# Kernel tuning notes

Hardware: AMD Instinct MI355X
Metric: run time of the kernel (lower is better)

Reference implementation:

```python
import jax, jax.numpy as jnp
import numpy as np

NSIDE = 64
NLAT = 4 * NSIDE - 1        # 255 iso-latitude rings
NLON = 4 * NSIDE            # 256 = max pixels per ring
NPIX = 12 * NSIDE * NSIDE   # 49152 HEALPix pixels
LMAX = NLAT                 # 255
MMAX = NLON // 2 + 1        # 129
BATCH, CHAN = 8, 32


def _ring_geometry():
    # HEALPix ring scheme: ring r (0-based), 1-based i=r+1
    #  north cap i<nside: nph=4i, phi shift 0.5
    #  equatorial nside<=i<=3*nside: nph=4*nside, shift alternates {0,0.5}
    #  south cap: mirror of north cap
    nph = np.zeros(NLAT, np.int64)
    shift = np.zeros(NLAT, np.float64)
    for r in range(NLAT):
        i = r + 1
        if i < NSIDE:
            nph[r], shift[r] = 4 * i, 0.5
        elif i <= 3 * NSIDE:
            nph[r], shift[r] = 4 * NSIDE, 0.5 * ((i - NSIDE + 1) % 2)
        else:
            nph[r], shift[r] = 4 * (NLAT - r), 0.5
    offs = np.concatenate([[0], np.cumsum(nph)[:-1]])
    p = np.arange(NLON)
    mask = (p[None, :] < nph[:, None])                       # [nlat, nlon]
    idx = (offs[:, None] + p[None, :]) * mask                # padded -> 0
    phase = 2.0 * np.pi * (p[None, :] + shift[:, None]) / nph[:, None] * mask
    return idx.astype(np.int32), mask.astype(np.float32), phase.astype(np.float32)


def setup_inputs() -> dict:
    key = jax.random.key(0)
    k1, k2, k3 = jax.random.split(key, 3)
    idx, mask, phase = _ring_geometry()
    x = jax.random.normal(k1, (BATCH, CHAN, NPIX), jnp.float32)
    pct = jax.random.normal(k2, (MMAX, LMAX, NLAT), jnp.float32) * 0.1  # Legendre table stand-in
    w = jax.random.uniform(k3, (NLAT,), jnp.float32)                    # per-ring quadrature weights
    return {"x": x, "pct": pct, "w": w,
            "ring_index": jnp.asarray(idx),
            "ring_mask": jnp.asarray(mask),
            "phase": jnp.asarray(phase)}


def _healpix_rfft_real(x, ring_index, ring_mask, phase):
    # x: [..., npix] -> per-ring DFT coefficients as real pairs [..., nlat, mmax, 2]
    rings = x[..., ring_index] * ring_mask                 # [..., nlat, nlon]
    m = jnp.arange(MMAX, dtype=phase.dtype)
    ang = phase[:, :, None] * m                            # [nlat, nlon, mmax]
    fr = jnp.einsum('...kp,kpm->...km', rings, jnp.cos(ang))
    fi = -jnp.einsum('...kp,kpm->...km', rings, jnp.sin(ang))
    return jnp.stack([fr, fi], axis=-1)                    # n=2 is view_as_real axis


def reference(x, pct, w, ring_index, ring_mask, phase):
    # healpix ring rFFT, then Legendre contraction (einsum '...kmn,mlk->...lmn')
    f = _healpix_rfft_real(x, ring_index, ring_mask, phase)  # [..., nlat, mmax, 2]
    weights = pct * w                                        # [mmax, lmax, nlat]
    out = jnp.einsum('...kmn,mlk->...lmn', f, weights)       # [..., lmax, mmax, 2]
    return out
```

## Files before the change

kernel.cpp:

```cpp
#include <hip/hip_runtime.h>

#define NLAT 255
#define NLON 256
#define NPIX 49152
#define MMAX 129
#define MCS  258
#define NTBL 65
#define TROWS 264

typedef unsigned short ushort_t;
typedef __attribute__((ext_vector_type(8)))  short  bf16x8;
typedef __attribute__((ext_vector_type(4)))  short  short4v;
typedef __attribute__((ext_vector_type(16))) float  f32x16;
typedef __attribute__((ext_vector_type(4)))  float  float4v;

__device__ __forceinline__ ushort_t f2bf(float f) {
    union { float f; unsigned u; } v; v.f = f;
    unsigned r = v.u + 0x7FFFu + ((v.u >> 16) & 1u);
    return (ushort_t)(r >> 16);
}
__device__ __forceinline__ float bf2f(ushort_t h) {
    union { unsigned u; float f; } v; v.u = ((unsigned)h) << 16;
    return v.f;
}

__global__ __launch_bounds__(256) void prepK(const float* __restrict__ pct,
                                             const float* __restrict__ w,
                                             ushort_t* __restrict__ pctw) {
    const int m  = blockIdx.x;
    const int l0 = blockIdx.y * 32;
    const int t  = threadIdx.x;
    const float wk = (t < NLAT) ? w[t] : 0.f;
    for (int l = l0; l < l0 + 32; ++l) {
        float v = 0.f;
        if (l < NLAT && t < NLAT)
            v = pct[((size_t)m * NLAT + l) * NLAT + t] * wk;
        pctw[((size_t)m * 256 + l) * 256 + t] = f2bf(v);
    }
}

__global__ __launch_bounds__(256) void trigK(const float* __restrict__ phase,
                                             const float* __restrict__ mask,
                                             ushort_t* __restrict__ Ttab2) {
    const int tt  = blockIdx.x;
    const int mcs = blockIdx.y;
    const int p   = threadIdx.x;
    const int r   = (tt < 63) ? tt : (tt == 63 ? 63 : 64);
    float val = 0.f;
    if (mcs < MCS) {
        float ph = phase[r * NLON + p];
        float mk = mask[r * NLON + p];
        float fm = (float)(mcs >> 1);
        float s, c;
        __sincosf(ph * fm, &s, &c);
        val = (mcs & 1) ? (-s * mk) : (c * mk);
    }
    Ttab2[(((size_t)tt * 4 + (p >> 6)) * TROWS + mcs) * 64 + (p & 63)] = f2bf(val);
}

__global__ __launch_bounds__(512, 2) void stageA(const float* __restrict__ x,
                                                 const int* __restrict__ ring_index,
                                                 const ushort_t* __restrict__ Ttab2,
                                                 ushort_t* __restrict__ f1) {
    __shared__ __align__(16) ushort_t Rs[256 * 72];
    __shared__ __align__(16) ushort_t Ts[TROWS * 72];

    const int r  = blockIdx.x;
    const int i1 = r + 1;
    const int nph = (i1 < 64) ? 4 * i1 : (i1 <= 192 ? 256 : 4 * (256 - i1));
    const int tbl = (i1 < 64) ? r : (i1 <= 192 ? (63 + (((i1 - 63) & 1) ^ 1)) : 254 - r);
    const int base = ring_index[r * NLON];

    const int t    = threadIdx.x;
    const int lane = t & 63;
    const int wid  = t >> 6;
    const int wrow = wid >> 1, wcol = wid & 1;
    const int lg   = lane >> 5;
    const int lc   = lane & 31;

    f32x16 acc[5][2];
#pragma unroll
    for (int tau = 0; tau < 5; ++tau)
#pragma unroll
        for (int i = 0; i < 2; ++i)
#pragma unroll
            for (int q = 0; q < 16; ++q) acc[tau][i][q] = 0.f;

    for (int pc = 0; pc < nph; pc += 64) {
        {
            const int p0 = (t & 15) * 4;
            const bool ok = (pc + p0) < nph;
#pragma unroll
            for (int pass = 0; pass < 8; ++pass) {
                int bc = (t >> 4) + pass * 32;
                float4v v = {0.f, 0.f, 0.f, 0.f};
                if (ok) v = *(const float4v*)(x + (size_t)bc * NPIX + base + pc + p0);
                short4v h;
                h[0] = (short)f2bf(v[0]); h[1] = (short)f2bf(v[1]);
                h[2] = (short)f2bf(v[2]); h[3] = (short)f2bf(v[3]);
                *(short4v*)(Rs + bc * 72 + p0) = h;
            }
        }
        {
            const ushort_t* slab = Ttab2 + ((size_t)tbl * 4 + (pc >> 6)) * (TROWS * 64);
#pragma unroll
            for (int pass = 0; pass < 5; ++pass) {
                int id = t + pass * 512;
                if (id < (TROWS * 64 / 8)) {
                    bf16x8 v = *(const bf16x8*)(slab + id * 8);
                    *(bf16x8*)(Ts + (id >> 3) * 72 + (id & 7) * 8) = v;
                }
            }
        }
        __syncthreads();
#pragma unroll
        for (int ks = 0; ks < 4; ++ks) {
            bf16x8 a0 = *(const bf16x8*)(Rs + (wrow * 64 + lc) * 72 + ks * 16 + lg * 8);
            bf16x8 a1 = *(const bf16x8*)(Rs + (wrow * 64 + 32 + lc) * 72 + ks * 16 + lg * 8);
#pragma unroll
            for (int tau = 0; tau < 5; ++tau) {
                int rr = tau * 64 + wcol * 32 + lc;
                int trow = rr > (TROWS - 1) ? (TROWS - 1) : rr;
                bf16x8 b = *(const bf16x8*)(Ts + trow * 72 + ks * 16 + lg * 8);
                acc[tau][0] = __builtin_amdgcn_mfma_f32_32x32x16_bf16(a0, b, acc[tau][0], 0, 0, 0);
                acc[tau][1] = __builtin_amdgcn_mfma_f32_32x32x16_bf16(a1, b, acc[tau][1], 0, 0, 0);
            }
        }
        __syncthreads();
    }

    ushort_t* Olds = Rs;
#pragma unroll
    for (int tau = 0; tau < 5; ++tau) {
        __syncthreads();
        {
            const int mcsl = wcol * 32 + lc;
#pragma unroll
            for (int i = 0; i < 2; ++i)
#pragma unroll
                for (int q = 0; q < 16; ++q) {
                    int bc = wrow * 64 + i * 32 + 4 * lg + (q & 3) + 8 * (q >> 2);
                    Olds[mcsl * 264 + bc] = f2bf(acc[tau][i][q]);
                }
        }
        __syncthreads();
#pragma unroll
        for (int it = 0; it < 4; ++it) {
            int row = (t >> 5) + it * 16;
            int ch  = t & 31;
            int mcs = tau * 64 + row;
            if (mcs < MCS) {
                bf16x8 v = *(const bf16x8*)(Olds + row * 264 + ch * 8);
                int m = mcs >> 1, n = mcs & 1;
                *(bf16x8*)(f1 + ((size_t)m * NLAT + r) * 512 + n * 256 + ch * 8) = v;
            }
        }
    }
}

__global__ __launch_bounds__(256) void transK(const ushort_t* __restrict__ f1,
                                              ushort_t* __restrict__ f1t, int m0) {
    __shared__ __align__(16) ushort_t T[64][72];
    const int m  = m0 + blockIdx.x;
    const int k0 = blockIdx.y * 64;
    const int b0 = blockIdx.z * 64;
    const int t  = threadIdx.x;
#pragma unroll
    for (int it = 0; it < 2; ++it) {
        int id = t + it * 256;
        int kk = id >> 3, ch = id & 7;
        int k  = k0 + kk;
        bf16x8 v = {0,0,0,0,0,0,0,0};
        if (k < NLAT)
            v = *(const bf16x8*)(f1 + ((size_t)m * NLAT + k) * 512 + b0 + ch * 8);
        *(bf16x8*)(&T[kk][ch * 8]) = v;
    }
    __syncthreads();
#pragma unroll
    for (int it = 0; it < 2; ++it) {
        int id  = t + it * 256;
        int bb  = id & 63, ch8 = id >> 6;
        bf16x8 v;
#pragma unroll
        for (int j = 0; j < 8; ++j) v[j] = T[ch8 * 8 + j][bb];
        *(bf16x8*)(f1t + ((size_t)m * 512 + b0 + bb) * 256 + k0 + ch8 * 8) = v;
    }
}

__global__ __launch_bounds__(256, 2) void stageB(const ushort_t* __restrict__ f1t,
                                                 const ushort_t* __restrict__ pctw,
                                                 ushort_t* __restrict__ otmp,
                                                 int mbase) {
    __shared__ __align__(16) ushort_t SB[30720];
    ushort_t* As = SB;
    ushort_t* Ws = SB + 10240;
    ushort_t* Es = SB;

    const int m   = mbase + (blockIdx.x >> 2);
    const int sub = blockIdx.x & 3;
    const int b2t = sub * 128;

    const int t     = threadIdx.x;
    const int lane  = t & 63;
    const int wid   = t >> 6;
    const int wrow  = wid >> 1, wlcol = wid & 1;
    const int lg    = lane >> 5, lc = lane & 31;

    f32x16 acc[2][4];
#pragma unroll
    for (int i = 0; i < 2; ++i)
#pragma unroll
        for (int j = 0; j < 4; ++j)
#pragma unroll
            for (int q = 0; q < 16; ++q) acc[i][j][q] = 0.f;

    auto fillA = [&](ushort_t* dst, int kc) {
#pragma unroll
        for (int pass = 0; pass < 2; ++pass) {
            int id  = t + pass * 256;
            int row = id >> 2, ch = id & 3;
            bf16x8 v = *(const bf16x8*)(f1t + ((size_t)m * 512 + b2t + row) * 256 + kc + ch * 8);
            *(bf16x8*)(dst + row * 40 + ch * 8) = v;
        }
    };
    auto fillW = [&](ushort_t* dst, int kc) {
#pragma unroll
        for (int pass = 0; pass < 4; ++pass) {
            int id  = t + pass * 256;
            int row = id >> 2, ch = id & 3;
            bf16x8 v = *(const bf16x8*)(pctw + ((size_t)m * 256 + row) * 256 + kc + ch * 8);
            *(bf16x8*)(dst + row * 40 + ch * 8) = v;
        }
    };

    fillA(As, 0);
    fillW(Ws, 0);
    __syncthreads();
    int buf = 0;
    for (int kc = 0; kc < 256; kc += 32, buf ^= 1) {
        if (kc + 32 < 256) {
            fillA(As + (buf ^ 1) * 5120, kc + 32);
            fillW(Ws + (buf ^ 1) * 10240, kc + 32);
        }
        const ushort_t* A = As + buf * 5120;
        const ushort_t* W = Ws + buf * 10240;
#pragma unroll
        for (int ks = 0; ks < 2; ++ks) {
            const int ko = ks * 16 + lg * 8;
            bf16x8 a0 = *(const bf16x8*)(A + (wrow * 64 + lc) * 40 + ko);
            bf16x8 a1 = *(const bf16x8*)(A + (wrow * 64 + 32 + lc) * 40 + ko);
#pragma unroll
            for (int jj = 0; jj < 4; ++jj) {
                bf16x8 b = *(const bf16x8*)(W + (wlcol * 128 + jj * 32 + lc) * 40 + ko);
                acc[0][jj] = __builtin_amdgcn_mfma_f32_32x32x16_bf16(a0, b, acc[0][jj], 0, 0, 0);
                acc[1][jj] = __builtin_amdgcn_mfma_f32_32x32x16_bf16(a1, b, acc[1][jj], 0, 0, 0);
            }
        }
        __syncthreads();
    }

#pragma unroll
    for (int h = 0; h < 2; ++h) {
        if (h) __syncthreads();
        if (wlcol == h) {
#pragma unroll
            for (int i = 0; i < 2; ++i)
#pragma unroll
                for (int jj = 0; jj < 4; ++jj)
#pragma unroll
                    for (int q = 0; q < 16; ++q) {
                        int bl = wrow * 64 + i * 32 + 4 * lg + (q & 3) + 8 * (q >> 2);
                        Es[bl * 136 + jj * 32 + lc] = f2bf(acc[i][jj][q]);
                    }
        }
        __syncthreads();
#pragma unroll
        for (int it = 0; it < 8; ++it) {
            int id  = t + it * 256;
            int row = id >> 4, ch = id & 15;
            bf16x8 v = *(const bf16x8*)(Es + row * 136 + ch * 8);
            *(bf16x8*)(otmp + (((size_t)m * 512 + b2t + row) << 8) + h * 128 + ch * 8) = v;
        }
    }
}

__global__ __launch_bounds__(256) void permuteK(const ushort_t* __restrict__ otmp,
                                                float* __restrict__ out) {
    __shared__ ushort_t L[MCS * 66];
    const int bc = blockIdx.x;
    const int l0 = blockIdx.y * 64;
    const int t  = threadIdx.x;
    const int ll = t & 63;
    const int l  = l0 + ll;
#pragma unroll 4
    for (int it = 0; it < 65; ++it) {
        int mn = (t >> 6) + it * 4;
        if (mn < MCS) {
            int mm = mn >> 1, n = mn & 1;
            ushort_t v = 0;
            if (l < NLAT)
                v = otmp[(((size_t)mm * 512 + n * 256 + bc) << 8) + l];
            L[mn * 66 + ll] = v;
        }
    }
    __syncthreads();
    for (int ll2 = 0; ll2 < 64; ++ll2) {
        int lo = l0 + ll2;
        if (lo >= NLAT) break;
        size_t rowb = ((size_t)bc * NLAT + lo) * MCS;
        out[rowb + t] = bf2f(L[t * 66 + ll2]);
        if (t < 2)
            out[rowb + 256 + t] = bf2f(L[(256 + t) * 66 + ll2]);
    }
}

extern "C" void kernel_launch(void* const* d_in, const int* in_sizes, int n_in,
                              void* d_out, int out_size, void* d_ws, size_t ws_size,
                              hipStream_t stream) {
    const float* x          = (const float*)d_in[0];
    const float* pct        = (const float*)d_in[1];
    const float* w          = (const float*)d_in[2];
    const int*   ring_index = (const int*)d_in[3];
    const float* ring_mask  = (const float*)d_in[4];
    const float* phase      = (const float*)d_in[5];
    float* out = (float*)d_out;

    char* wsb = (char*)d_ws;
    ushort_t* f1    = (ushort_t*)wsb;
    ushort_t* Ttab2 = (ushort_t*)(wsb + 33684480);
    ushort_t* f1t   = (ushort_t*)(wsb + 33552384);
    ushort_t* otmp  = (ushort_t*)wsb;
    ushort_t* pctw  = (ushort_t*)d_out;

    prepK   <<<dim3(MMAX, 8),   256, 0, stream>>>(pct, w, pctw);
    trigK   <<<dim3(NTBL, TROWS), 256, 0, stream>>>(phase, ring_mask, Ttab2);
    stageA  <<<dim3(NLAT),      512, 0, stream>>>(x, ring_index, Ttab2, f1);
    transK  <<<dim3(1, 4, 8),   256, 0, stream>>>(f1, f1t, 128);
    transK  <<<dim3(128, 4, 8), 256, 0, stream>>>(f1, f1t, 0);
    stageB  <<<dim3(256),       256, 0, stream>>>(f1t, pctw, otmp, 0);
    stageB  <<<dim3(260),       256, 0, stream>>>(f1t, pctw, otmp, 64);
    permuteK<<<dim3(256, 4),    256, 0, stream>>>(otmp, out);
}
```

Before: 142.4 us.

## Split stageA across batch-channel tiles with swizzled trig table and direct LDS loads

StageA now launches 4x more blocks, each handling 64 of the 256 batch-channel rows for one ring, with 256 threads and a smaller per-block accumulator. The goal is more parallelism and occupancy beyond the 255 ring blocks. The trig table is written in an XOR-swizzled layout so it can be copied straight into LDS with global_load_lds, with no padding and no register round trip, while still avoiding bank conflicts. The cost is that each trig slab is now loaded four times, once per batch tile, which adds global and L2 traffic.

```diff
diff --git a/kernel.cpp b/kernel.cpp
--- a/kernel.cpp
+++ b/kernel.cpp
@@ -55,17 +55,20 @@
         __sincosf(ph * fm, &s, &c);
         val = (mcs & 1) ? (-s * mk) : (c * mk);
     }
-    Ttab2[(((size_t)tt * 4 + (p >> 6)) * TROWS + mcs) * 64 + (p & 63)] = f2bf(val);
-}
-
-__global__ __launch_bounds__(512, 2) void stageA(const float* __restrict__ x,
+    const int pl  = p & 63;
+    const int swz = ((((pl >> 3) ^ mcs) & 7) << 3) | (pl & 7);
+    Ttab2[(((size_t)tt * 4 + (p >> 6)) * TROWS + mcs) * 64 + swz] = f2bf(val);
+}
+
+__global__ __launch_bounds__(256, 3) void stageA(const float* __restrict__ x,
                                                  const int* __restrict__ ring_index,
                                                  const ushort_t* __restrict__ Ttab2,
                                                  ushort_t* __restrict__ f1) {
-    __shared__ __align__(16) ushort_t Rs[256 * 72];
-    __shared__ __align__(16) ushort_t Ts[TROWS * 72];
-
-    const int r  = blockIdx.x;
+    __shared__ __align__(16) ushort_t Rs[64 * 72];
+    __shared__ __align__(16) ushort_t Ts[TROWS * 64];
+
+    const int b0 = blockIdx.x * 64;
+    const int r  = blockIdx.y;
     const int i1 = r + 1;
     const int nph = (i1 < 64) ? 4 * i1 : (i1 <= 192 ? 256 : 4 * (256 - i1));
     const int tbl = (i1 < 64) ? r : (i1 <= 192 ? (63 + (((i1 - 63) & 1) ^ 1)) : 254 - r);
@@ -78,23 +81,21 @@
     const int lg   = lane >> 5;
     const int lc   = lane & 31;
 
-    f32x16 acc[5][2];
+    f32x16 acc[5];
 #pragma unroll
     for (int tau = 0; tau < 5; ++tau)
 #pragma unroll
-        for (int i = 0; i < 2; ++i)
-#pragma unroll
-            for (int q = 0; q < 16; ++q) acc[tau][i][q] = 0.f;
+        for (int q = 0; q < 16; ++q) acc[tau][q] = 0.f;
 
     for (int pc = 0; pc < nph; pc += 64) {
         {
             const int p0 = (t & 15) * 4;
             const bool ok = (pc + p0) < nph;
 #pragma unroll
-            for (int pass = 0; pass < 8; ++pass) {
-                int bc = (t >> 4) + pass * 32;
+            for (int pass = 0; pass < 4; ++pass) {
+                int bc = (t >> 4) + pass * 16;
                 float4v v = {0.f, 0.f, 0.f, 0.f};
-                if (ok) v = *(const float4v*)(x + (size_t)bc * NPIX + base + pc + p0);
+                if (ok) v = *(const float4v*)(x + (size_t)(b0 + bc) * NPIX + base + pc + p0);
                 short4v h;
                 h[0] = (short)f2bf(v[0]); h[1] = (short)f2bf(v[1]);
                 h[2] = (short)f2bf(v[2]); h[3] = (short)f2bf(v[3]);
@@ -103,27 +104,24 @@
         }
         {
             const ushort_t* slab = Ttab2 + ((size_t)tbl * 4 + (pc >> 6)) * (TROWS * 64);
-#pragma unroll
-            for (int pass = 0; pass < 5; ++pass) {
-                int id = t + pass * 512;
-                if (id < (TROWS * 64 / 8)) {
-                    bf16x8 v = *(const bf16x8*)(slab + id * 8);
-                    *(bf16x8*)(Ts + (id >> 3) * 72 + (id & 7) * 8) = v;
-                }
+            for (int s = wid; s < 33; s += 4) {
+                __builtin_amdgcn_global_load_lds(
+                    (const __attribute__((address_space(1))) void*)(slab + s * 512 + lane * 8),
+                    (__attribute__((address_space(3))) void*)(Ts + s * 512),
+                    16, 0, 0);
             }
         }
         __syncthreads();
 #pragma unroll
         for (int ks = 0; ks < 4; ++ks) {
-            bf16x8 a0 = *(const bf16x8*)(Rs + (wrow * 64 + lc) * 72 + ks * 16 + lg * 8);
-            bf16x8 a1 = *(const bf16x8*)(Rs + (wrow * 64 + 32 + lc) * 72 + ks * 16 + lg * 8);
+            bf16x8 a = *(const bf16x8*)(Rs + (wrow * 32 + lc) * 72 + ks * 16 + lg * 8);
+            const int c = ks * 2 + lg;
 #pragma unroll
             for (int tau = 0; tau < 5; ++tau) {
-                int rr = tau * 64 + wcol * 32 + lc;
+                int rr   = tau * 64 + wcol * 32 + lc;
                 int trow = rr > (TROWS - 1) ? (TROWS - 1) : rr;
-                bf16x8 b = *(const bf16x8*)(Ts + trow * 72 + ks * 16 + lg * 8);
-                acc[tau][0] = __builtin_amdgcn_mfma_f32_32x32x16_bf16(a0, b, acc[tau][0], 0, 0, 0);
-                acc[tau][1] = __builtin_amdgcn_mfma_f32_32x32x16_bf16(a1, b, acc[tau][1], 0, 0, 0);
+                bf16x8 b = *(const bf16x8*)(Ts + trow * 64 + ((c ^ (trow & 7)) << 3));
+                acc[tau] = __builtin_amdgcn_mfma_f32_32x32x16_bf16(a, b, acc[tau], 0, 0, 0);
             }
         }
         __syncthreads();
@@ -136,23 +134,23 @@
         {
             const int mcsl = wcol * 32 + lc;
 #pragma unroll
-            for (int i = 0; i < 2; ++i)
-#pragma unroll
-                for (int q = 0; q < 16; ++q) {
-                    int bc = wrow * 64 + i * 32 + 4 * lg + (q & 3) + 8 * (q >> 2);
-                    Olds[mcsl * 264 + bc] = f2bf(acc[tau][i][q]);
-                }
-        }
-        __syncthreads();
-#pragma unroll
-        for (int it = 0; it < 4; ++it) {
-            int row = (t >> 5) + it * 16;
-            int ch  = t & 31;
+            for (int q = 0; q < 16; ++q) {
+                int bcl = wrow * 32 + 4 * lg + (q & 3) + 8 * (q >> 2);
+                Olds[mcsl * 72 + bcl] = f2bf(acc[tau][q]);
+            }
+        }
+        __syncthreads();
+        {
+            int row = t >> 2;
             int mcs = tau * 64 + row;
             if (mcs < MCS) {
-                bf16x8 v = *(const bf16x8*)(Olds + row * 264 + ch * 8);
                 int m = mcs >> 1, n = mcs & 1;
-                *(bf16x8*)(f1 + ((size_t)m * NLAT + r) * 512 + n * 256 + ch * 8) = v;
+                size_t gbase = ((size_t)m * NLAT + r) * 512 + n * 256 + b0 + (t & 3) * 16;
+#pragma unroll
+                for (int j = 0; j < 2; ++j) {
+                    bf16x8 v = *(const bf16x8*)(Olds + row * 72 + (t & 3) * 16 + j * 8);
+                    *(bf16x8*)(f1 + gbase + j * 8) = v;
+                }
             }
         }
     }
@@ -332,12 +330,12 @@
     ushort_t* otmp  = (ushort_t*)wsb;
     ushort_t* pctw  = (ushort_t*)d_out;
 
-    prepK   <<<dim3(MMAX, 8),   256, 0, stream>>>(pct, w, pctw);
+    prepK   <<<dim3(MMAX, 8),     256, 0, stream>>>(pct, w, pctw);
     trigK   <<<dim3(NTBL, TROWS), 256, 0, stream>>>(phase, ring_mask, Ttab2);
-    stageA  <<<dim3(NLAT),      512, 0, stream>>>(x, ring_index, Ttab2, f1);
-    transK  <<<dim3(1, 4, 8),   256, 0, stream>>>(f1, f1t, 128);
-    transK  <<<dim3(128, 4, 8), 256, 0, stream>>>(f1, f1t, 0);
-    stageB  <<<dim3(256),       256, 0, stream>>>(f1t, pctw, otmp, 0);
-    stageB  <<<dim3(260),       256, 0, stream>>>(f1t, pctw, otmp, 64);
-    permuteK<<<dim3(256, 4),    256, 0, stream>>>(otmp, out);
-}
+    stageA  <<<dim3(4, NLAT),     256, 0, stream>>>(x, ring_index, Ttab2, f1);
+    transK  <<<dim3(1, 4, 8),     256, 0, stream>>>(f1, f1t, 128);
+    transK  <<<dim3(128, 4, 8),   256, 0, stream>>>(f1, f1t, 0);
+    stageB  <<<dim3(256),         256, 0, stream>>>(f1t, pctw, otmp, 0);
+    stageB  <<<dim3(260),         256, 0, stream>>>(f1t, pctw, otmp, 64);
+    permuteK<<<dim3(256, 4),      256, 0, stream>>>(otmp, out);
+}
```

New measurement: 142.8 us. Within noise of the previous version (+0.2%).
